# Kernel optimization log

Measured on AMD Instinct MI355X. Metric: run time of the kernel, lower is better.

## Reference

```python
import jax, jax.numpy as jnp
import numpy as np

N0, N1, N2 = 250000, 200000, 150000
N = N0 + N1 + N2  # total nodes
H = 128           # hidden_dim
FEAT_DIMS = (64, 128, 256)


def setup_inputs() -> dict:
    key = jax.random.key(0)
    ks = jax.random.split(key, 8)
    # disjoint per-type node index sets (equivalent to np.where(type_mask == i))
    perm = jax.random.permutation(ks[0], N)
    idx0 = jnp.sort(perm[:N0])
    idx1 = jnp.sort(perm[N0:N0 + N1])
    idx2 = jnp.sort(perm[N0 + N1:])
    x0 = jax.random.normal(ks[1], (N0, FEAT_DIMS[0]), dtype=jnp.float32)
    x1 = jax.random.normal(ks[2], (N1, FEAT_DIMS[1]), dtype=jnp.float32)
    x2 = jax.random.normal(ks[3], (N2, FEAT_DIMS[2]), dtype=jnp.float32)
    # torch nn.Linear weights: [out, in], xavier-normal-ish scale
    def lin(k, din):
        kw, kb = jax.random.split(k)
        scale = 1.414 * (2.0 / (din + H)) ** 0.5
        W = jax.random.normal(kw, (H, din), dtype=jnp.float32) * scale
        b = jax.random.uniform(kb, (H,), dtype=jnp.float32, minval=-1.0, maxval=1.0) / (din ** 0.5)
        return W, b
    W0, b0 = lin(ks[4], FEAT_DIMS[0])
    W1, b1 = lin(ks[5], FEAT_DIMS[1])
    W2, b2 = lin(ks[6], FEAT_DIMS[2])
    return {"x0": x0, "x1": x1, "x2": x2,
            "W0": W0, "b0": b0, "W1": W1, "b1": b1, "W2": W2, "b2": b2,
            "idx0": idx0, "idx1": idx1, "idx2": idx2}


def reference(x0, x1, x2, W0, b0, W1, b1, W2, b2, idx0, idx1, idx2):
    # per-type Linear (y = x W^T + b) then scatter into zero-initialized [N, H]
    n_nodes = idx0.shape[0] + idx1.shape[0] + idx2.shape[0]
    out = jnp.zeros((n_nodes, W0.shape[0]), dtype=x0.dtype)
    out = out.at[idx0].set(x0 @ W0.T + b0)
    out = out.at[idx1].set(x1 @ W1.T + b1)
    out = out.at[idx2].set(x2 @ W2.T + b2)
    return out  # transformed_features (dropout_rate=0 -> identity)
```

## Files before the change

kernel.cpp:

```cpp
#include <hip/hip_runtime.h>

typedef __bf16 bf16x8 __attribute__((ext_vector_type(8)));
typedef float f32x4 __attribute__((ext_vector_type(4)));

__global__ void prep_all_kernel(const float* __restrict__ W0, const float* __restrict__ W1,
                                const float* __restrict__ W2,
                                __bf16* __restrict__ Bf0, __bf16* __restrict__ Bf1,
                                __bf16* __restrict__ Bf2) {
    int t = blockIdx.x * blockDim.x + threadIdx.x;
    const float* W;
    __bf16* dst;
    int K;
    if (t < 1024)      { W = W0; dst = Bf0; K = 64; }
    else if (t < 3072) { W = W1; dst = Bf1; K = 128; t -= 1024; }
    else if (t < 7168) { W = W2; dst = Bf2; K = 256; t -= 3072; }
    else return;
    int lane = t & 63;
    int hf = (t >> 6) & 7;
    int ks = t >> 9;
    int row = hf * 16 + (lane & 15);
    int k0 = ks * 32 + ((lane >> 4) << 3);
    const float* src = W + (size_t)row * K + k0;
    __bf16* d = dst + (size_t)t * 8;
#pragma unroll
    for (int e = 0; e < 8; ++e) d[e] = (__bf16)src[e];
}

template <int K>
__device__ __forceinline__ void run_type(
    const float* __restrict__ x, const __bf16* __restrict__ Wfrag,
    const float* __restrict__ bias, const int* __restrict__ idx,
    float* __restrict__ out, int M, int blk)
{
    constexpr int KSTEPS = K / 32;
    const int lane = threadIdx.x & 63;
    const int wave = threadIdx.x >> 6;
    const int l15 = lane & 15;
    const int kg = lane >> 4;
    const int rowbase = blk * 128 + wave * 32;

    const int gr0 = rowbase + l15;
    const int gr1 = gr0 + 16;
    const int r0c = gr0 < M ? gr0 : M - 1;
    const int r1c = gr1 < M ? gr1 : M - 1;
    const int orow0 = idx[r0c];
    const int orow1 = idx[r1c];

    const float* a0p = x + (size_t)r0c * K + kg * 8;
    const float* a1p = x + (size_t)r1c * K + kg * 8;
    const bf16x8* wbase = reinterpret_cast<const bf16x8*>(Wfrag) + lane;

    f32x4 acc[2][8] = {};

#pragma unroll
    for (int ks = 0; ks < KSTEPS; ++ks) {
        bf16x8 xf0, xf1;
        {
            f32x4 u0 = *reinterpret_cast<const f32x4*>(a0p + ks * 32);
            f32x4 u1 = *reinterpret_cast<const f32x4*>(a0p + ks * 32 + 4);
            f32x4 v0 = *reinterpret_cast<const f32x4*>(a1p + ks * 32);
            f32x4 v1 = *reinterpret_cast<const f32x4*>(a1p + ks * 32 + 4);
            xf0[0] = (__bf16)u0[0]; xf0[1] = (__bf16)u0[1]; xf0[2] = (__bf16)u0[2]; xf0[3] = (__bf16)u0[3];
            xf0[4] = (__bf16)u1[0]; xf0[5] = (__bf16)u1[1]; xf0[6] = (__bf16)u1[2]; xf0[7] = (__bf16)u1[3];
            xf1[0] = (__bf16)v0[0]; xf1[1] = (__bf16)v0[1]; xf1[2] = (__bf16)v0[2]; xf1[3] = (__bf16)v0[3];
            xf1[4] = (__bf16)v1[0]; xf1[5] = (__bf16)v1[1]; xf1[6] = (__bf16)v1[2]; xf1[7] = (__bf16)v1[3];
        }
        bf16x8 w[8];
#pragma unroll
        for (int hf = 0; hf < 8; ++hf) w[hf] = wbase[(ks * 8 + hf) * 64];
#pragma unroll
        for (int hf = 0; hf < 8; ++hf) {
            acc[0][hf] = __builtin_amdgcn_mfma_f32_16x16x32_bf16(w[hf], xf0, acc[0][hf], 0, 0, 0);
            acc[1][hf] = __builtin_amdgcn_mfma_f32_16x16x32_bf16(w[hf], xf1, acc[1][hf], 0, 0, 0);
        }
    }

#pragma unroll
    for (int hf = 0; hf < 8; ++hf) {
        f32x4 bv = *reinterpret_cast<const f32x4*>(bias + hf * 16 + kg * 4);
        if (gr0 < M) {
            f32x4 v = acc[0][hf] + bv;
            *reinterpret_cast<f32x4*>(out + (size_t)orow0 * 128 + hf * 16 + kg * 4) = v;
        }
        if (gr1 < M) {
            f32x4 v = acc[1][hf] + bv;
            *reinterpret_cast<f32x4*>(out + (size_t)orow1 * 128 + hf * 16 + kg * 4) = v;
        }
    }
}

__global__ __launch_bounds__(256, 3) void fused_linear_kernel(
    const float* __restrict__ x0, const float* __restrict__ x1, const float* __restrict__ x2,
    const __bf16* __restrict__ Bf0, const __bf16* __restrict__ Bf1, const __bf16* __restrict__ Bf2,
    const float* __restrict__ b0, const float* __restrict__ b1, const float* __restrict__ b2,
    const int* __restrict__ idx0, const int* __restrict__ idx1, const int* __restrict__ idx2,
    float* __restrict__ out, int M0, int M1, int M2, int nb2, int nb21)
{
    int b = blockIdx.x;
    if (b < nb2)       run_type<256>(x2, Bf2, b2, idx2, out, M2, b);
    else if (b < nb21) run_type<128>(x1, Bf1, b1, idx1, out, M1, b - nb2);
    else               run_type<64>(x0, Bf0, b0, idx0, out, M0, b - nb21);
}

extern "C" void kernel_launch(void* const* d_in, const int* in_sizes, int n_in,
                              void* d_out, int out_size, void* d_ws, size_t ws_size,
                              hipStream_t stream) {
    const float* x0 = (const float*)d_in[0];
    const float* x1 = (const float*)d_in[1];
    const float* x2 = (const float*)d_in[2];
    const float* W0 = (const float*)d_in[3];
    const float* b0 = (const float*)d_in[4];
    const float* W1 = (const float*)d_in[5];
    const float* b1 = (const float*)d_in[6];
    const float* W2 = (const float*)d_in[7];
    const float* b2 = (const float*)d_in[8];
    const int* idx0 = (const int*)d_in[9];
    const int* idx1 = (const int*)d_in[10];
    const int* idx2 = (const int*)d_in[11];
    float* out = (float*)d_out;

    const int M0 = in_sizes[9];
    const int M1 = in_sizes[10];
    const int M2 = in_sizes[11];

    __bf16* Bf0 = (__bf16*)d_ws;
    __bf16* Bf1 = Bf0 + 2 * 8 * 64 * 8;
    __bf16* Bf2 = Bf1 + 4 * 8 * 64 * 8;

    prep_all_kernel<<<(7168 + 255) / 256, 256, 0, stream>>>(W0, W1, W2, Bf0, Bf1, Bf2);

    const int nb0 = (M0 + 127) / 128;
    const int nb1 = (M1 + 127) / 128;
    const int nb2 = (M2 + 127) / 128;
    fused_linear_kernel<<<nb0 + nb1 + nb2, 256, 0, stream>>>(
        x0, x1, x2, Bf0, Bf1, Bf2, b0, b1, b2, idx0, idx1, idx2,
        out, M0, M1, M2, nb2, nb2 + nb1);
}
```

Measured before the change: 164.2 us.

## Stage activations through LDS with async global_load_lds triple-buffer pipeline

Replaces the direct per-lane global loads of x with asynchronous global-to-LDS copies into a swizzled, per-wave triple buffer. Each wave keeps two k-steps in flight, waiting on vmcnt before reading the current buffer from LDS and converting it to bf16 for the MFMAs. The goal is to overlap activation fetch latency with compute and to get fully coalesced row loads. In exchange it adds 48KB of LDS per block, which can limit occupancy, plus manual scheduling barriers and waitcnt tuning that make correctness depend on exact vmcnt accounting.

```diff
diff --git a/kernel.cpp b/kernel.cpp
--- a/kernel.cpp
+++ b/kernel.cpp
@@ -2,6 +2,12 @@
 
 typedef __bf16 bf16x8 __attribute__((ext_vector_type(8)));
 typedef float f32x4 __attribute__((ext_vector_type(4)));
+
+__device__ __forceinline__ void gload_lds16(const float* g, float* l) {
+    __builtin_amdgcn_global_load_lds(
+        (const __attribute__((address_space(1))) void*)g,
+        (__attribute__((address_space(3))) void*)l, 16, 0, 0);
+}
 
 __global__ void prep_all_kernel(const float* __restrict__ W0, const float* __restrict__ W1,
                                 const float* __restrict__ W2,
@@ -30,44 +36,72 @@
 __device__ __forceinline__ void run_type(
     const float* __restrict__ x, const __bf16* __restrict__ Wfrag,
     const float* __restrict__ bias, const int* __restrict__ idx,
-    float* __restrict__ out, int M, int blk)
+    float* __restrict__ out, int M, int blk,
+    float (&lds)[3][4][32][32])
 {
     constexpr int KSTEPS = K / 32;
     const int lane = threadIdx.x & 63;
     const int wave = threadIdx.x >> 6;
     const int l15 = lane & 15;
     const int kg = lane >> 4;
-    const int rowbase = blk * 128 + wave * 32;
+    const int wavebase = blk * 128 + wave * 32;
 
-    const int gr0 = rowbase + l15;
+    const int gr0 = wavebase + l15;
     const int gr1 = gr0 + 16;
     const int r0c = gr0 < M ? gr0 : M - 1;
     const int r1c = gr1 < M ? gr1 : M - 1;
-    const int orow0 = idx[r0c];
-    const int orow1 = idx[r1c];
+    int orow0 = idx[r0c];
+    int orow1 = idx[r1c];
+    asm volatile("" : "+v"(orow0), "+v"(orow1));
 
-    const float* a0p = x + (size_t)r0c * K + kg * 8;
-    const float* a1p = x + (size_t)r1c * K + kg * 8;
+    const float* gstage[4];
+#pragma unroll
+    for (int j = 0; j < 4; ++j) {
+        int srow = j * 8 + (lane >> 3);
+        int grow = wavebase + srow;
+        grow = grow < M ? grow : M - 1;
+        int usw = ((lane & 7) ^ ((lane >> 3) & 7)) << 2;
+        gstage[j] = x + (size_t)grow * K + usw;
+    }
+
     const bf16x8* wbase = reinterpret_cast<const bf16x8*>(Wfrag) + lane;
+    const int u0 = (2 * kg) ^ (l15 & 7);
 
     f32x4 acc[2][8] = {};
 
 #pragma unroll
-    for (int ks = 0; ks < KSTEPS; ++ks) {
-        bf16x8 xf0, xf1;
-        {
-            f32x4 u0 = *reinterpret_cast<const f32x4*>(a0p + ks * 32);
-            f32x4 u1 = *reinterpret_cast<const f32x4*>(a0p + ks * 32 + 4);
-            f32x4 v0 = *reinterpret_cast<const f32x4*>(a1p + ks * 32);
-            f32x4 v1 = *reinterpret_cast<const f32x4*>(a1p + ks * 32 + 4);
-            xf0[0] = (__bf16)u0[0]; xf0[1] = (__bf16)u0[1]; xf0[2] = (__bf16)u0[2]; xf0[3] = (__bf16)u0[3];
-            xf0[4] = (__bf16)u1[0]; xf0[5] = (__bf16)u1[1]; xf0[6] = (__bf16)u1[2]; xf0[7] = (__bf16)u1[3];
-            xf1[0] = (__bf16)v0[0]; xf1[1] = (__bf16)v0[1]; xf1[2] = (__bf16)v0[2]; xf1[3] = (__bf16)v0[3];
-            xf1[4] = (__bf16)v1[0]; xf1[5] = (__bf16)v1[1]; xf1[6] = (__bf16)v1[2]; xf1[7] = (__bf16)v1[3];
-        }
+    for (int j = 0; j < 4; ++j) gload_lds16(gstage[j] + 0 * 32, &lds[0][wave][j * 8][0]);
+#pragma unroll
+    for (int j = 0; j < 4; ++j) gload_lds16(gstage[j] + 1 * 32, &lds[1][wave][j * 8][0]);
+    __builtin_amdgcn_sched_barrier(0);
+    asm volatile("s_waitcnt vmcnt(4)" ::: "memory");
+    __builtin_amdgcn_sched_barrier(0);
+
+#pragma unroll 1
+    for (int i = 0; i < KSTEPS; ++i) {
+        const int buf = i % 3;
+        f32x4 p0 = *(const f32x4*)&lds[buf][wave][l15][u0 * 4];
+        f32x4 p1 = *(const f32x4*)&lds[buf][wave][l15][(u0 ^ 1) * 4];
+        f32x4 q0 = *(const f32x4*)&lds[buf][wave][l15 + 16][u0 * 4];
+        f32x4 q1 = *(const f32x4*)&lds[buf][wave][l15 + 16][(u0 ^ 1) * 4];
+        __builtin_amdgcn_sched_barrier(0);
         bf16x8 w[8];
 #pragma unroll
-        for (int hf = 0; hf < 8; ++hf) w[hf] = wbase[(ks * 8 + hf) * 64];
+        for (int hf = 0; hf < 8; ++hf) w[hf] = wbase[(i * 8 + hf) * 64];
+        __builtin_amdgcn_sched_barrier(0);
+        const int ksn = (i + 2 < KSTEPS) ? i + 2 : KSTEPS - 1;
+        const int bufn = (i + 2) % 3;
+#pragma unroll
+        for (int j = 0; j < 4; ++j)
+            gload_lds16(gstage[j] + ksn * 32, &lds[bufn][wave][j * 8][0]);
+        __builtin_amdgcn_sched_barrier(0);
+        asm volatile("s_waitcnt vmcnt(4)" ::: "memory");
+        __builtin_amdgcn_sched_barrier(0);
+        bf16x8 xf0, xf1;
+        xf0[0] = (__bf16)p0[0]; xf0[1] = (__bf16)p0[1]; xf0[2] = (__bf16)p0[2]; xf0[3] = (__bf16)p0[3];
+        xf0[4] = (__bf16)p1[0]; xf0[5] = (__bf16)p1[1]; xf0[6] = (__bf16)p1[2]; xf0[7] = (__bf16)p1[3];
+        xf1[0] = (__bf16)q0[0]; xf1[1] = (__bf16)q0[1]; xf1[2] = (__bf16)q0[2]; xf1[3] = (__bf16)q0[3];
+        xf1[4] = (__bf16)q1[0]; xf1[5] = (__bf16)q1[1]; xf1[6] = (__bf16)q1[2]; xf1[7] = (__bf16)q1[3];
 #pragma unroll
         for (int hf = 0; hf < 8; ++hf) {
             acc[0][hf] = __builtin_amdgcn_mfma_f32_16x16x32_bf16(w[hf], xf0, acc[0][hf], 0, 0, 0);
@@ -96,10 +130,11 @@
     const int* __restrict__ idx0, const int* __restrict__ idx1, const int* __restrict__ idx2,
     float* __restrict__ out, int M0, int M1, int M2, int nb2, int nb21)
 {
+    __shared__ float lds[3][4][32][32];
     int b = blockIdx.x;
-    if (b < nb2)       run_type<256>(x2, Bf2, b2, idx2, out, M2, b);
-    else if (b < nb21) run_type<128>(x1, Bf1, b1, idx1, out, M1, b - nb2);
-    else               run_type<64>(x0, Bf0, b0, idx0, out, M0, b - nb21);
+    if (b < nb2)       run_type<256>(x2, Bf2, b2, idx2, out, M2, b, lds);
+    else if (b < nb21) run_type<128>(x1, Bf1, b1, idx1, out, M1, b - nb2, lds);
+    else               run_type<64>(x0, Bf0, b0, idx0, out, M0, b - nb21, lds);
 }
 
 extern "C" void kernel_launch(void* const* d_in, const int* in_sizes, int n_in,
```

Result: no change. 166.5 us (+1.4%).

## Stage x rows into LDS via direct global-to-LDS loads with swizzle and double-buffered weights

Applied to the files above, without the earlier changes.

Each wave now handles 16 rows instead of 32. It issues its activation tile as asynchronous global_load_lds 16-byte transfers into a per-wave LDS buffer with an XOR swizzle, then reads fragments from LDS. Weight fragments are double-buffered across k-steps, with explicit vmcnt waits to overlap loads with MFMA. Blocks shrink to 128 threads covering 32 rows, so there are four times as many blocks. The aim is better latency hiding and coalesced loads, at the cost of more weight-fragment reloads per row and the hand-tuned waitcnt ordering.

```diff
diff --git a/kernel.cpp b/kernel.cpp
--- a/kernel.cpp
+++ b/kernel.cpp
@@ -2,6 +2,12 @@
 
 typedef __bf16 bf16x8 __attribute__((ext_vector_type(8)));
 typedef float f32x4 __attribute__((ext_vector_type(4)));
+
+__device__ __forceinline__ void gload_lds16(const float* g, float* l) {
+    __builtin_amdgcn_global_load_lds(
+        (const __attribute__((address_space(1))) void*)g,
+        (__attribute__((address_space(3))) void*)l, 16, 0, 0);
+}
 
 __global__ void prep_all_kernel(const float* __restrict__ W0, const float* __restrict__ W1,
                                 const float* __restrict__ W2,
@@ -30,76 +36,91 @@
 __device__ __forceinline__ void run_type(
     const float* __restrict__ x, const __bf16* __restrict__ Wfrag,
     const float* __restrict__ bias, const int* __restrict__ idx,
-    float* __restrict__ out, int M, int blk)
+    float* __restrict__ out, int M, int blk, float* ldsw)
 {
     constexpr int KSTEPS = K / 32;
+    constexpr int UPR = K / 4;
+    constexpr int LUPR = (K == 256) ? 6 : (K == 128 ? 5 : 4);
+    constexpr int NST = (16 * UPR) / 64;
     const int lane = threadIdx.x & 63;
     const int wave = threadIdx.x >> 6;
     const int l15 = lane & 15;
     const int kg = lane >> 4;
-    const int rowbase = blk * 128 + wave * 32;
+    const int wrb = blk * 32 + wave * 16;
 
-    const int gr0 = rowbase + l15;
-    const int gr1 = gr0 + 16;
+    const int gr0 = wrb + l15;
     const int r0c = gr0 < M ? gr0 : M - 1;
-    const int r1c = gr1 < M ? gr1 : M - 1;
-    const int orow0 = idx[r0c];
-    const int orow1 = idx[r1c];
-
-    const float* a0p = x + (size_t)r0c * K + kg * 8;
-    const float* a1p = x + (size_t)r1c * K + kg * 8;
-    const bf16x8* wbase = reinterpret_cast<const bf16x8*>(Wfrag) + lane;
-
-    f32x4 acc[2][8] = {};
+    int orow0 = idx[r0c];
+    asm volatile("" : "+v"(orow0));
 
 #pragma unroll
-    for (int ks = 0; ks < KSTEPS; ++ks) {
-        bf16x8 xf0, xf1;
-        {
-            f32x4 u0 = *reinterpret_cast<const f32x4*>(a0p + ks * 32);
-            f32x4 u1 = *reinterpret_cast<const f32x4*>(a0p + ks * 32 + 4);
-            f32x4 v0 = *reinterpret_cast<const f32x4*>(a1p + ks * 32);
-            f32x4 v1 = *reinterpret_cast<const f32x4*>(a1p + ks * 32 + 4);
-            xf0[0] = (__bf16)u0[0]; xf0[1] = (__bf16)u0[1]; xf0[2] = (__bf16)u0[2]; xf0[3] = (__bf16)u0[3];
-            xf0[4] = (__bf16)u1[0]; xf0[5] = (__bf16)u1[1]; xf0[6] = (__bf16)u1[2]; xf0[7] = (__bf16)u1[3];
-            xf1[0] = (__bf16)v0[0]; xf1[1] = (__bf16)v0[1]; xf1[2] = (__bf16)v0[2]; xf1[3] = (__bf16)v0[3];
-            xf1[4] = (__bf16)v1[0]; xf1[5] = (__bf16)v1[1]; xf1[6] = (__bf16)v1[2]; xf1[7] = (__bf16)v1[3];
+    for (int s = 0; s < NST; ++s) {
+        int f = s * 64 + lane;
+        int row = f >> LUPR;
+        int unit = f & (UPR - 1);
+        int su = unit ^ (row & 7);
+        int grow = wrb + row;
+        grow = grow < M ? grow : M - 1;
+        gload_lds16(x + (size_t)grow * K + su * 4, ldsw + s * 256);
+    }
+    __builtin_amdgcn_sched_barrier(0);
+
+    const bf16x8* wbase = reinterpret_cast<const bf16x8*>(Wfrag) + lane;
+    bf16x8 w[2][8];
+#pragma unroll
+    for (int hf = 0; hf < 8; ++hf) w[0][hf] = wbase[hf * 64];
+    __builtin_amdgcn_sched_barrier(0);
+
+    f32x4 acc[8] = {};
+    const float* lrow = ldsw + l15 * K;
+
+#pragma unroll
+    for (int i = 0; i < KSTEPS; ++i) {
+        if (i + 1 < KSTEPS) {
+#pragma unroll
+            for (int hf = 0; hf < 8; ++hf) w[(i + 1) & 1][hf] = wbase[((i + 1) * 8 + hf) * 64];
+            __builtin_amdgcn_sched_barrier(0);
+            asm volatile("s_waitcnt vmcnt(8)" ::: "memory");
+        } else {
+            __builtin_amdgcn_sched_barrier(0);
+            asm volatile("s_waitcnt vmcnt(0)" ::: "memory");
         }
-        bf16x8 w[8];
+        __builtin_amdgcn_sched_barrier(0);
+        const int u0 = (i * 8 + 2 * kg) ^ (l15 & 7);
+        const int u1 = (i * 8 + 2 * kg + 1) ^ (l15 & 7);
+        f32x4 p0 = *(const f32x4*)(lrow + u0 * 4);
+        f32x4 p1 = *(const f32x4*)(lrow + u1 * 4);
+        bf16x8 xf;
+        xf[0] = (__bf16)p0[0]; xf[1] = (__bf16)p0[1]; xf[2] = (__bf16)p0[2]; xf[3] = (__bf16)p0[3];
+        xf[4] = (__bf16)p1[0]; xf[5] = (__bf16)p1[1]; xf[6] = (__bf16)p1[2]; xf[7] = (__bf16)p1[3];
 #pragma unroll
-        for (int hf = 0; hf < 8; ++hf) w[hf] = wbase[(ks * 8 + hf) * 64];
+        for (int hf = 0; hf < 8; ++hf)
+            acc[hf] = __builtin_amdgcn_mfma_f32_16x16x32_bf16(w[i & 1][hf], xf, acc[hf], 0, 0, 0);
+    }
+
+    if (gr0 < M) {
 #pragma unroll
         for (int hf = 0; hf < 8; ++hf) {
-            acc[0][hf] = __builtin_amdgcn_mfma_f32_16x16x32_bf16(w[hf], xf0, acc[0][hf], 0, 0, 0);
-            acc[1][hf] = __builtin_amdgcn_mfma_f32_16x16x32_bf16(w[hf], xf1, acc[1][hf], 0, 0, 0);
-        }
-    }
-
-#pragma unroll
-    for (int hf = 0; hf < 8; ++hf) {
-        f32x4 bv = *reinterpret_cast<const f32x4*>(bias + hf * 16 + kg * 4);
-        if (gr0 < M) {
-            f32x4 v = acc[0][hf] + bv;
+            f32x4 bv = *reinterpret_cast<const f32x4*>(bias + hf * 16 + kg * 4);
+            f32x4 v = acc[hf] + bv;
             *reinterpret_cast<f32x4*>(out + (size_t)orow0 * 128 + hf * 16 + kg * 4) = v;
-        }
-        if (gr1 < M) {
-            f32x4 v = acc[1][hf] + bv;
-            *reinterpret_cast<f32x4*>(out + (size_t)orow1 * 128 + hf * 16 + kg * 4) = v;
         }
     }
 }
 
-__global__ __launch_bounds__(256, 3) void fused_linear_kernel(
+__global__ __launch_bounds__(128, 2) void fused_linear_kernel(
     const float* __restrict__ x0, const float* __restrict__ x1, const float* __restrict__ x2,
     const __bf16* __restrict__ Bf0, const __bf16* __restrict__ Bf1, const __bf16* __restrict__ Bf2,
     const float* __restrict__ b0, const float* __restrict__ b1, const float* __restrict__ b2,
     const int* __restrict__ idx0, const int* __restrict__ idx1, const int* __restrict__ idx2,
     float* __restrict__ out, int M0, int M1, int M2, int nb2, int nb21)
 {
+    __shared__ float lds[2][4096];
     int b = blockIdx.x;
-    if (b < nb2)       run_type<256>(x2, Bf2, b2, idx2, out, M2, b);
-    else if (b < nb21) run_type<128>(x1, Bf1, b1, idx1, out, M1, b - nb2);
-    else               run_type<64>(x0, Bf0, b0, idx0, out, M0, b - nb21);
+    float* ldsw = lds[threadIdx.x >> 6];
+    if (b < nb2)       run_type<256>(x2, Bf2, b2, idx2, out, M2, b, ldsw);
+    else if (b < nb21) run_type<128>(x1, Bf1, b1, idx1, out, M1, b - nb2, ldsw);
+    else               run_type<64>(x0, Bf0, b0, idx0, out, M0, b - nb21, ldsw);
 }
 
 extern "C" void kernel_launch(void* const* d_in, const int* in_sizes, int n_in,
@@ -129,10 +150,10 @@
 
     prep_all_kernel<<<(7168 + 255) / 256, 256, 0, stream>>>(W0, W1, W2, Bf0, Bf1, Bf2);
 
-    const int nb0 = (M0 + 127) / 128;
-    const int nb1 = (M1 + 127) / 128;
-    const int nb2 = (M2 + 127) / 128;
-    fused_linear_kernel<<<nb0 + nb1 + nb2, 256, 0, stream>>>(
+    const int nb0 = (M0 + 31) / 32;
+    const int nb1 = (M1 + 31) / 32;
+    const int nb2 = (M2 + 31) / 32;
+    fused_linear_kernel<<<nb0 + nb1 + nb2, 128, 0, stream>>>(
         x0, x1, x2, Bf0, Bf1, Bf2, b0, b1, b2, idx0, idx1, idx2,
         out, M0, M1, M2, nb2, nb2 + nb1);
 }
```

Measured after the change: 177.6 us. 1.08x slower.

## Stage weight fragments in LDS via direct global-to-LDS loads and prefetch X

Applied to the files above, without the earlier changes.

Weight fragments are now copied cooperatively into a 32KB shared buffer with global_load_lds. For K=256 this happens in two phases, and each wave then reads its MFMA operands from LDS instead of issuing per-wave global loads. X row loads are software-pipelined two k-steps ahead through a triple-buffered register array. This is meant to cut redundant L2 weight traffic and hide X load latency. In exchange it adds block barriers, 32KB of LDS per block that may limit occupancy, and more register pressure.

```diff
diff --git a/kernel.cpp b/kernel.cpp
--- a/kernel.cpp
+++ b/kernel.cpp
@@ -2,6 +2,12 @@
 
 typedef __bf16 bf16x8 __attribute__((ext_vector_type(8)));
 typedef float f32x4 __attribute__((ext_vector_type(4)));
+
+__device__ __forceinline__ void gload_lds16(const void* g, void* l) {
+    __builtin_amdgcn_global_load_lds(
+        (const __attribute__((address_space(1))) void*)g,
+        (__attribute__((address_space(3))) void*)l, 16, 0, 0);
+}
 
 __global__ void prep_all_kernel(const float* __restrict__ W0, const float* __restrict__ W1,
                                 const float* __restrict__ W2,
@@ -30,11 +36,17 @@
 __device__ __forceinline__ void run_type(
     const float* __restrict__ x, const __bf16* __restrict__ Wfrag,
     const float* __restrict__ bias, const int* __restrict__ idx,
-    float* __restrict__ out, int M, int blk)
+    float* __restrict__ out, int M, int blk, __bf16* ldsW)
 {
     constexpr int KSTEPS = K / 32;
-    const int lane = threadIdx.x & 63;
-    const int wave = threadIdx.x >> 6;
+    constexpr int PHASES = (K == 256) ? 2 : 1;
+    constexpr int KSP = KSTEPS / PHASES;
+    constexpr int PHASE_BYTES = KSP * 8 * 64 * 16;
+    constexpr int NST = PHASE_BYTES / (256 * 16);
+
+    const int tid = threadIdx.x;
+    const int lane = tid & 63;
+    const int wave = tid >> 6;
     const int l15 = lane & 15;
     const int kg = lane >> 4;
     const int rowbase = blk * 128 + wave * 32;
@@ -43,35 +55,66 @@
     const int gr1 = gr0 + 16;
     const int r0c = gr0 < M ? gr0 : M - 1;
     const int r1c = gr1 < M ? gr1 : M - 1;
-    const int orow0 = idx[r0c];
-    const int orow1 = idx[r1c];
+    int orow0 = idx[r0c];
+    int orow1 = idx[r1c];
+    asm volatile("" : "+v"(orow0), "+v"(orow1));
 
     const float* a0p = x + (size_t)r0c * K + kg * 8;
     const float* a1p = x + (size_t)r1c * K + kg * 8;
-    const bf16x8* wbase = reinterpret_cast<const bf16x8*>(Wfrag) + lane;
+
+    f32x4 xs[3][4];
+    auto ldx = [&](int i) {
+        int ii = i < KSTEPS ? i : KSTEPS - 1;
+        f32x4* s = xs[i % 3];
+        s[0] = *(const f32x4*)(a0p + ii * 32);
+        s[1] = *(const f32x4*)(a0p + ii * 32 + 4);
+        s[2] = *(const f32x4*)(a1p + ii * 32);
+        s[3] = *(const f32x4*)(a1p + ii * 32 + 4);
+    };
+
+    auto stageW = [&](int ph) {
+        const char* src = (const char*)Wfrag + (size_t)ph * PHASE_BYTES;
+        char* dst = (char*)ldsW;
+#pragma unroll
+        for (int s = 0; s < NST; ++s)
+            gload_lds16(src + (s * 256 + tid) * 16, dst + (s * 256 + tid) * 16);
+    };
 
     f32x4 acc[2][8] = {};
 
+    ldx(0);
+    ldx(1);
+    stageW(0);
+    asm volatile("s_waitcnt vmcnt(0)" ::: "memory");
+    __builtin_amdgcn_sched_barrier(0);
+    __syncthreads();
+
 #pragma unroll
-    for (int ks = 0; ks < KSTEPS; ++ks) {
-        bf16x8 xf0, xf1;
-        {
-            f32x4 u0 = *reinterpret_cast<const f32x4*>(a0p + ks * 32);
-            f32x4 u1 = *reinterpret_cast<const f32x4*>(a0p + ks * 32 + 4);
-            f32x4 v0 = *reinterpret_cast<const f32x4*>(a1p + ks * 32);
-            f32x4 v1 = *reinterpret_cast<const f32x4*>(a1p + ks * 32 + 4);
-            xf0[0] = (__bf16)u0[0]; xf0[1] = (__bf16)u0[1]; xf0[2] = (__bf16)u0[2]; xf0[3] = (__bf16)u0[3];
-            xf0[4] = (__bf16)u1[0]; xf0[5] = (__bf16)u1[1]; xf0[6] = (__bf16)u1[2]; xf0[7] = (__bf16)u1[3];
-            xf1[0] = (__bf16)v0[0]; xf1[1] = (__bf16)v0[1]; xf1[2] = (__bf16)v0[2]; xf1[3] = (__bf16)v0[3];
-            xf1[4] = (__bf16)v1[0]; xf1[5] = (__bf16)v1[1]; xf1[6] = (__bf16)v1[2]; xf1[7] = (__bf16)v1[3];
+    for (int p = 0; p < PHASES; ++p) {
+        if (p > 0) {
+            __syncthreads();
+            stageW(p);
+            asm volatile("s_waitcnt vmcnt(0)" ::: "memory");
+            __builtin_amdgcn_sched_barrier(0);
+            __syncthreads();
         }
-        bf16x8 w[8];
 #pragma unroll
-        for (int hf = 0; hf < 8; ++hf) w[hf] = wbase[(ks * 8 + hf) * 64];
+        for (int j = 0; j < KSP; ++j) {
+            const int i = p * KSP + j;
+            ldx(i + 2);
+            const f32x4* cu = xs[i % 3];
+            bf16x8 xf0, xf1;
+            xf0[0] = (__bf16)cu[0][0]; xf0[1] = (__bf16)cu[0][1]; xf0[2] = (__bf16)cu[0][2]; xf0[3] = (__bf16)cu[0][3];
+            xf0[4] = (__bf16)cu[1][0]; xf0[5] = (__bf16)cu[1][1]; xf0[6] = (__bf16)cu[1][2]; xf0[7] = (__bf16)cu[1][3];
+            xf1[0] = (__bf16)cu[2][0]; xf1[1] = (__bf16)cu[2][1]; xf1[2] = (__bf16)cu[2][2]; xf1[3] = (__bf16)cu[2][3];
+            xf1[4] = (__bf16)cu[3][0]; xf1[5] = (__bf16)cu[3][1]; xf1[6] = (__bf16)cu[3][2]; xf1[7] = (__bf16)cu[3][3];
+            const __bf16* wl = ldsW + ((size_t)j * 8 * 64 + lane) * 8;
 #pragma unroll
-        for (int hf = 0; hf < 8; ++hf) {
-            acc[0][hf] = __builtin_amdgcn_mfma_f32_16x16x32_bf16(w[hf], xf0, acc[0][hf], 0, 0, 0);
-            acc[1][hf] = __builtin_amdgcn_mfma_f32_16x16x32_bf16(w[hf], xf1, acc[1][hf], 0, 0, 0);
+            for (int hf = 0; hf < 8; ++hf) {
+                bf16x8 w = *(const bf16x8*)(wl + (size_t)hf * 64 * 8);
+                acc[0][hf] = __builtin_amdgcn_mfma_f32_16x16x32_bf16(w, xf0, acc[0][hf], 0, 0, 0);
+                acc[1][hf] = __builtin_amdgcn_mfma_f32_16x16x32_bf16(w, xf1, acc[1][hf], 0, 0, 0);
+            }
         }
     }
 
@@ -96,10 +139,11 @@
     const int* __restrict__ idx0, const int* __restrict__ idx1, const int* __restrict__ idx2,
     float* __restrict__ out, int M0, int M1, int M2, int nb2, int nb21)
 {
+    __shared__ __bf16 ldsW[16384];
     int b = blockIdx.x;
-    if (b < nb2)       run_type<256>(x2, Bf2, b2, idx2, out, M2, b);
-    else if (b < nb21) run_type<128>(x1, Bf1, b1, idx1, out, M1, b - nb2);
-    else               run_type<64>(x0, Bf0, b0, idx0, out, M0, b - nb21);
+    if (b < nb2)       run_type<256>(x2, Bf2, b2, idx2, out, M2, b, ldsW);
+    else if (b < nb21) run_type<128>(x1, Bf1, b1, idx1, out, M1, b - nb2, ldsW);
+    else               run_type<64>(x0, Bf0, b0, idx0, out, M0, b - nb21, ldsW);
 }
 
 extern "C" void kernel_launch(void* const* d_in, const int* in_sizes, int n_in,
```

Result: slower. 168.7 us (+2.7%).
